# Kernel optimization log

Hardware: AMD Instinct MI355X
Metric: run time of the kernel (lower is better)

Reference implementation:

```python
import jax, jax.numpy as jnp
import numpy as np

HEADS = 8
DIM_HEAD = 64
QUERY_DIM = 1024
CONTEXT_DIM = 768
INNER = HEADS * DIM_HEAD  # 512


def setup_inputs() -> dict:
    key = jax.random.key(0)
    ks = jax.random.split(key, 7)
    B, Sq, Skv = 4, 4096, 1024
    x = jax.random.normal(ks[0], (B, Sq, QUERY_DIM), dtype=jnp.float32)
    context = jax.random.normal(ks[1], (B, Skv, CONTEXT_DIM), dtype=jnp.float32)
    # nn.Linear(in, out) weights stored as [out, in]; we use [in, out] for x @ W
    Wq = jax.random.normal(ks[2], (QUERY_DIM, INNER), dtype=jnp.float32) * (QUERY_DIM ** -0.5)
    Wk = jax.random.normal(ks[3], (CONTEXT_DIM, INNER), dtype=jnp.float32) * (CONTEXT_DIM ** -0.5)
    Wv = jax.random.normal(ks[4], (CONTEXT_DIM, INNER), dtype=jnp.float32) * (CONTEXT_DIM ** -0.5)
    Wo = jax.random.normal(ks[5], (INNER, QUERY_DIM), dtype=jnp.float32) * (INNER ** -0.5)
    bo = jax.random.normal(ks[6], (QUERY_DIM,), dtype=jnp.float32) * 0.01
    return {"x": x, "context": context, "Wq": Wq, "Wk": Wk, "Wv": Wv, "Wo": Wo, "bo": bo}


def reference(x, context, Wq, Wk, Wv, Wo, bo):
    B, Sq, _ = x.shape
    h, d = HEADS, DIM_HEAD
    scale = d ** -0.5
    # project and split heads: [B, S, h*d] -> [B, h, S, d]
    q = (x @ Wq).reshape(B, Sq, h, d).transpose(0, 2, 1, 3)
    k = (context @ Wk).reshape(B, -1, h, d).transpose(0, 2, 1, 3)
    v = (context @ Wv).reshape(B, -1, h, d).transpose(0, 2, 1, 3)
    # the torch chunked loop is exactly full softmax attention (softmax is row-wise)
    scores = jnp.einsum('bhid,bhjd->bhij', q, k) * scale
    attn = jax.nn.softmax(scores, axis=-1)
    out = jnp.einsum('bhij,bhjd->bhid', attn, v)  # [B, h, Sq, d]
    out = out.transpose(0, 2, 1, 3).reshape(B, Sq, h * d)
    return out @ Wo + bo
```

## Files before the change

### kernel.cpp

```cpp
#include <hip/hip_runtime.h>

#define SQ 4096
#define SKV 1024
#define BATCH 4
#define NH 8
#define DH 64
#define QD 1024
#define CD 768
#define INNER 512

typedef _Float16 half8 __attribute__((ext_vector_type(8)));
typedef _Float16 half4v __attribute__((ext_vector_type(4)));
typedef float floatx4 __attribute__((ext_vector_type(4)));
typedef float f32x16 __attribute__((ext_vector_type(16)));
typedef unsigned int uint4v __attribute__((ext_vector_type(4)));

#define MFMA16(a, b, c) __builtin_amdgcn_mfma_f32_16x16x32_f16(a, b, c, 0, 0, 0)
#define MFMA32(a, b, c) __builtin_amdgcn_mfma_f32_32x32x16_f16(a, b, c, 0, 0, 0)

#define PLSWAP(a, b) asm("v_permlane32_swap_b32 %0, %1" : "+v"(a), "+v"(b))

#define GLD16(gptr, lptr)                                                            \
  __builtin_amdgcn_global_load_lds(                                                  \
      (const __attribute__((address_space(1))) unsigned int*)(const void*)(gptr),    \
      (__attribute__((address_space(3))) unsigned int*)(void*)(lptr), 16, 0, 0)

__global__ __launch_bounds__(256) void transpose_all(const float* __restrict__ Wq,
                                                     const float* __restrict__ Wk,
                                                     const float* __restrict__ Wv,
                                                     const float* __restrict__ Wo,
                                                     _Float16* __restrict__ wqt,
                                                     _Float16* __restrict__ wkvt,
                                                     _Float16* __restrict__ wot) {
  __shared__ float tile[32][33];
  const int z = blockIdx.z;
  const float* src; _Float16* dst; int R, C;
  if (z == 0)      { src = Wq; dst = wqt;                        R = QD;    C = INNER; }
  else if (z == 1) { src = Wk; dst = wkvt;                       R = CD;    C = INNER; }
  else if (z == 2) { src = Wv; dst = wkvt + (size_t)INNER * CD;  R = CD;    C = INNER; }
  else             { src = Wo; dst = wot;                        R = INNER; C = QD;   }
  const int c0 = blockIdx.x * 32, r0 = blockIdx.y * 32;
  if (c0 >= C || r0 >= R) return;
  const int tx = threadIdx.x & 31, ty = threadIdx.x >> 5;
#pragma unroll
  for (int i = 0; i < 32; i += 8)
    tile[ty + i][tx] = src[(size_t)(r0 + ty + i) * C + c0 + tx];
  __syncthreads();
#pragma unroll
  for (int i = 0; i < 32; i += 8)
    dst[(size_t)(c0 + ty + i) * R + r0 + tx] = (_Float16)tile[tx][ty + i];
}

template <int MODE, int AF32>
__device__ __forceinline__ void gemm_body(const void* __restrict__ Aany,
                                          const _Float16* __restrict__ Bt,
                                          void* __restrict__ Cout,
                                          void* __restrict__ Cout2,
                                          const float* __restrict__ bias,
                                          int M, int N, int K, int bx, int by,
                                          void* AsRaw, _Float16* Bs) {
  float* As32 = (float*)AsRaw;
  _Float16* As16 = (_Float16*)AsRaw;
  const int tid = threadIdx.x;
  const int wave = tid >> 6, lane = tid & 63;
  const int quad = lane >> 4, l16 = lane & 15;
  const int wm = (wave >> 1) * 64, wn = (wave & 1) * 64;
  const size_t n0 = (size_t)bx * 128, m0 = (size_t)by * 128;

  floatx4 acc[4][4] = {};

  const float* a32g = (const float*)Aany + (m0 + (tid >> 3)) * (size_t)K + (tid & 7) * 4;
  const _Float16* a16g = (const _Float16*)Aany + (m0 + (tid >> 2)) * (size_t)K + (tid & 3) * 8;
  const _Float16* bg = Bt + (n0 + (tid >> 2)) * (size_t)K + (tid & 3) * 8;

#define GSTAGE(bi, k0)                                                        \
  do {                                                                        \
    if (AF32) {                                                               \
      GLD16(a32g + (k0), As32 + (bi)*4096 + tid * 4);                         \
      GLD16(a32g + (k0) + (size_t)32 * K, As32 + (bi)*4096 + tid * 4 + 1024); \
      GLD16(a32g + (k0) + (size_t)64 * K, As32 + (bi)*4096 + tid * 4 + 2048); \
      GLD16(a32g + (k0) + (size_t)96 * K, As32 + (bi)*4096 + tid * 4 + 3072); \
    } else {                                                                  \
      GLD16(a16g + (k0), As16 + (bi)*4096 + tid * 8);                         \
      GLD16(a16g + (k0) + (size_t)64 * K, As16 + (bi)*4096 + tid * 8 + 2048); \
    }                                                                         \
    GLD16(bg + (k0), Bs + (bi)*4096 + tid * 8);                               \
    GLD16(bg + (k0) + (size_t)64 * K, Bs + (bi)*4096 + tid * 8 + 2048);       \
  } while (0)

  const int NT = K / 32;
  GSTAGE(0, 0);
  for (int t = 0; t < NT; ++t) {
    __syncthreads();
    if (t + 1 < NT) GSTAGE((t + 1) & 1, (t + 1) * 32);
    const int bo = (t & 1) * 4096;

    half8 af[4], bf[4];
#pragma unroll
    for (int mt = 0; mt < 4; ++mt) {
      const int row = wm + mt * 16 + l16;
      if (AF32) {
        floatx4 x0 = *(const floatx4*)(As32 + bo + row * 32 + quad * 8);
        floatx4 x1 = *(const floatx4*)(As32 + bo + row * 32 + quad * 8 + 4);
        half8 tt;
#pragma unroll
        for (int i = 0; i < 4; ++i) { tt[i] = (_Float16)x0[i]; tt[4 + i] = (_Float16)x1[i]; }
        af[mt] = tt;
      } else {
        af[mt] = *(const half8*)(As16 + bo + row * 32 + quad * 8);
      }
    }
#pragma unroll
    for (int nt = 0; nt < 4; ++nt)
      bf[nt] = *(const half8*)(Bs + bo + (wn + nt * 16 + l16) * 32 + quad * 8);
    __builtin_amdgcn_s_setprio(1);
#pragma unroll
    for (int mt = 0; mt < 4; ++mt)
#pragma unroll
      for (int nt = 0; nt < 4; ++nt)
        acc[mt][nt] = MFMA16(af[mt], bf[nt], acc[mt][nt]);
    __builtin_amdgcn_s_setprio(0);
  }
#undef GSTAGE

  if (MODE == 3) {
    _Float16* C = (_Float16*)Cout;
    const float sc = 0.125f * 1.44269504088896f;
#pragma unroll
    for (int mt = 0; mt < 4; ++mt) {
      const size_t row = m0 + wm + mt * 16 + quad * 4;
#pragma unroll
      for (int nt = 0; nt < 4; ++nt) {
        const size_t col = n0 + wn + nt * 16 + l16;
#pragma unroll
        for (int r = 0; r < 4; ++r)
          C[(row + r) * N + col] = (_Float16)(acc[mt][nt][r] * sc);
      }
    }
  } else if (MODE == 4) {
    if (n0 < INNER) {
      _Float16* C = (_Float16*)Cout;
#pragma unroll
      for (int mt = 0; mt < 4; ++mt) {
        const size_t row = m0 + wm + mt * 16 + quad * 4;
#pragma unroll
        for (int nt = 0; nt < 4; ++nt) {
          const size_t col = n0 + wn + nt * 16 + l16;
#pragma unroll
          for (int r = 0; r < 4; ++r)
            C[(row + r) * INNER + col] = (_Float16)acc[mt][nt][r];
        }
      }
    } else {
      _Float16* C = (_Float16*)Cout2;
      const int b = (int)(m0 >> 10);
#pragma unroll
      for (int mt = 0; mt < 4; ++mt) {
        const int kvb = (int)(m0 & 1023) + wm + mt * 16 + quad * 4;
#pragma unroll
        for (int nt = 0; nt < 4; ++nt) {
          const int col = (int)(n0 - INNER + wn + nt * 16 + l16);
          const int h = col >> 6, d = col & 63;
          half4v pk;
#pragma unroll
          for (int r = 0; r < 4; ++r) pk[r] = (_Float16)acc[mt][nt][r];
          *(half4v*)(C + (size_t)((b * NH + h) * DH + d) * SKV + kvb) = pk;
        }
      }
    }
  } else {
    float* C = (float*)Cout;
#pragma unroll
    for (int mt = 0; mt < 4; ++mt) {
      const size_t row = m0 + wm + mt * 16 + quad * 4;
#pragma unroll
      for (int nt = 0; nt < 4; ++nt) {
        const size_t col = n0 + wn + nt * 16 + l16;
        const float bb = bias[col];
#pragma unroll
        for (int r = 0; r < 4; ++r)
          C[(row + r) * N + col] = acc[mt][nt][r] + bb;
      }
    }
  }
}

__global__ __launch_bounds__(256) void proj_fused(const float* __restrict__ x,
                                                  const float* __restrict__ ctx,
                                                  const _Float16* __restrict__ wqt,
                                                  const _Float16* __restrict__ wkvt,
                                                  _Float16* __restrict__ qh,
                                                  _Float16* __restrict__ kh,
                                                  _Float16* __restrict__ vth) {
  __shared__ float As32[2 * 128 * 32];
  __shared__ _Float16 Bs[2 * 128 * 32];
  const int b = blockIdx.x;
  const int xcd = b & 7, j = b >> 3;
  const int seg = j % 3;
  if (seg == 2) {
    const int jkv = j / 3;
    gemm_body<4, 1>((const void*)ctx, wkvt, kh, vth, nullptr, BATCH * SKV,
                    2 * INNER, CD, jkv & 7, xcd * 4 + (jkv >> 3), As32, Bs);
  } else {
    const int jq = (j / 3) * 2 + seg;
    gemm_body<3, 1>((const void*)x, wqt, qh, nullptr, nullptr, BATCH * SQ,
                    INNER, QD, jq & 3, xcd * 16 + (jq >> 2), As32, Bs);
  }
}

__global__ __launch_bounds__(256) void gemm_out(const _Float16* __restrict__ A,
                                                const _Float16* __restrict__ Bt,
                                                float* __restrict__ Cout,
                                                const float* __restrict__ bias) {
  __shared__ _Float16 As16[2 * 128 * 32];
  __shared__ _Float16 Bs[2 * 128 * 32];
  const int b = blockIdx.x;
  const int xcd = b & 7, i = b >> 3;
  gemm_body<2, 0>((const void*)A, Bt, Cout, nullptr, bias, BATCH * SQ, QD, INNER,
                  i & 7, xcd * 16 + (i >> 3), As16, Bs);
}

__global__ __launch_bounds__(256, 3) void flash_attn8(const _Float16* __restrict__ Q,
                                                      const _Float16* __restrict__ Kp,
                                                      const _Float16* __restrict__ Vt,
                                                      _Float16* __restrict__ O) {
  __shared__ _Float16 Ksb[2 * 64 * 64];
  __shared__ _Float16 Vsb[2 * 64 * 64];
  const int tid = threadIdx.x;
  const int wave = tid >> 6, lane = tid & 63;
  const int l31 = lane & 31, hi = lane >> 5, x7 = lane & 7;

  const int flat = blockIdx.x;
  const int nf = (flat & 7) * 128 + (flat >> 3);
  const int qblk = nf & 31, bh = nf >> 5;
  const int b = bh >> 3, h = bh & 7;

  const size_t qrow0 = (size_t)b * SQ + qblk * 128 + wave * 32;
  const _Float16* qptr = Q + qrow0 * INNER + h * DH;
  const _Float16* kbase = Kp + (size_t)b * SKV * INNER + h * DH;
  const _Float16* vbase = Vt + (size_t)bh * DH * SKV;

  const int kr = tid >> 3;
  const int kb = (tid & 7) ^ (kr & 7);
  const _Float16* kg = kbase + (size_t)kr * INNER + kb * 8;
  const _Float16* vg = vbase + (size_t)kr * SKV + kb * 8;

#define STAGE_KV(bi, tt)                                                        \
  do {                                                                          \
    _Float16* _kl = Ksb + (bi) * 4096 + tid * 8;                                \
    _Float16* _vl = Vsb + (bi) * 4096 + tid * 8;                                \
    GLD16(kg + (size_t)((tt) * 64) * INNER, _kl);                               \
    GLD16(kg + (size_t)((tt) * 64 + 32) * INNER, _kl + 2048);                   \
    GLD16(vg + (tt) * 64, _vl);                                                 \
    GLD16(vg + (size_t)32 * SKV + (tt) * 64, _vl + 2048);                       \
  } while (0)

  half8 aq[4];
#pragma unroll
  for (int i = 0; i < 4; ++i)
    aq[i] = *(const half8*)(qptr + (size_t)l31 * INNER + i * 16 + hi * 8);

  int koff[4], voffB[4];
#pragma unroll
  for (int i = 0; i < 4; ++i)
    koff[i] = l31 * 64 + (((i * 2 + hi) ^ x7) << 3);
#pragma unroll
  for (int j = 0; j < 4; ++j)
    voffB[j] = l31 * 64 + (((j * 2 + hi) ^ x7) << 3);

  half8 ones;
#pragma unroll
  for (int j = 0; j < 8; ++j) ones[j] = (_Float16)1.0f;

  f32x16 o0 = {}, o1 = {}, osum = {};

  STAGE_KV(0, 0);

  for (int t = 0; t < SKV / 64; ++t) {
    __syncthreads();
    if (t < SKV / 64 - 1) STAGE_KV((t + 1) & 1, t + 1);
    const _Float16* ks = Ksb + (t & 1) * 4096;
    const _Float16* vs = Vsb + (t & 1) * 4096;

#pragma unroll
    for (int c2 = 0; c2 < 2; ++c2) {
      half8 ak[4];
#pragma unroll
      for (int i = 0; i < 4; ++i)
        ak[i] = *(const half8*)(ks + c2 * 2048 + koff[i]);

      f32x16 st = {};
#pragma unroll
      for (int i = 0; i < 4; ++i) st = MFMA32(ak[i], aq[i], st);

      unsigned w[8];
#pragma unroll
      for (int j = 0; j < 8; ++j) {
        float plo = __builtin_exp2f(st[2 * j]);
        float phi = __builtin_exp2f(st[2 * j + 1]);
        w[j] = __builtin_bit_cast(unsigned, __builtin_amdgcn_cvt_pkrtz(plo, phi));
      }
      PLSWAP(w[0], w[2]);
      PLSWAP(w[1], w[3]);
      PLSWAP(w[4], w[6]);
      PLSWAP(w[5], w[7]);
      uint4v u0 = {w[0], w[1], w[2], w[3]};
      uint4v u1 = {w[4], w[5], w[6], w[7]};
      half8 A0 = __builtin_bit_cast(half8, u0);
      half8 A1 = __builtin_bit_cast(half8, u1);

      osum = MFMA32(A0, ones, osum);
      osum = MFMA32(A1, ones, osum);

      {
        half8 bv00 = *(const half8*)(vs + 0 * 2048 + voffB[c2 * 2 + 0]);
        half8 bv10 = *(const half8*)(vs + 1 * 2048 + voffB[c2 * 2 + 0]);
        o0 = MFMA32(A0, bv00, o0);
        o1 = MFMA32(A0, bv10, o1);
        half8 bv01 = *(const half8*)(vs + 0 * 2048 + voffB[c2 * 2 + 1]);
        half8 bv11 = *(const half8*)(vs + 1 * 2048 + voffB[c2 * 2 + 1]);
        o0 = MFMA32(A1, bv01, o0);
        o1 = MFMA32(A1, bv11, o1);
      }
    }
  }

  float inv16[16];
#pragma unroll
  for (int r = 0; r < 16; ++r) inv16[r] = 1.0f / osum[r];

  _Float16* op = O + qrow0 * INNER + h * DH;
#pragma unroll
  for (int r = 0; r < 16; ++r) {
    const int q = (r & 3) + 8 * (r >> 2) + 4 * hi;
    op[(size_t)q * INNER + l31] = (_Float16)(o0[r] * inv16[r]);
    op[(size_t)q * INNER + 32 + l31] = (_Float16)(o1[r] * inv16[r]);
  }
#undef STAGE_KV
}

extern "C" void kernel_launch(void* const* d_in, const int* in_sizes, int n_in,
                              void* d_out, int out_size, void* d_ws, size_t ws_size,
                              hipStream_t stream) {
  const float* x   = (const float*)d_in[0];
  const float* ctx = (const float*)d_in[1];
  const float* Wq  = (const float*)d_in[2];
  const float* Wk  = (const float*)d_in[3];
  const float* Wv  = (const float*)d_in[4];
  const float* Wo  = (const float*)d_in[5];
  const float* bo  = (const float*)d_in[6];
  float* out = (float*)d_out;

  _Float16* ws = (_Float16*)d_ws;
  _Float16* wqt  = ws;
  _Float16* wkvt = wqt + (size_t)INNER * QD;
  _Float16* wot  = wkvt + (size_t)2 * INNER * CD;
  _Float16* qh   = wot + (size_t)QD * INNER;
  _Float16* kh   = qh + (size_t)BATCH * SQ * INNER;
  _Float16* vth  = kh + (size_t)BATCH * SKV * INNER;
  _Float16* aoh  = vth + (size_t)BATCH * SKV * INNER;

  transpose_all<<<dim3(32, 32, 4), 256, 0, stream>>>(Wq, Wk, Wv, Wo, wqt, wkvt, wot);

  proj_fused<<<dim3(768), 256, 0, stream>>>(x, ctx, wqt, wkvt, qh, kh, vth);

  flash_attn8<<<dim3(BATCH * NH * SQ / 128), 256, 0, stream>>>(qh, kh, vth, aoh);

  gemm_out<<<dim3(1024), 256, 0, stream>>>(aoh, wot, out, bo);
}
```

Before: 255.6 us.

## Replace LDS-staged projection GEMMs with direct global-to-register loads

The projection and output GEMMs drop their double-buffered shared-memory staging (global_load_lds plus barriers) and instead load MFMA fragments straight from global memory into registers, unrolling the K loop by two. N and K become template constants, and the launch bounds now request 3 blocks per SM. The aim is to remove LDS traffic and __syncthreads overhead and raise occupancy. In exchange, each wave issues strided, poorly coalesced global loads with no sharing across waves, so it leans heavily on L1/L2 and loses the latency hiding that the explicit double buffer provided.

```diff
diff --git a/kernel.cpp b/kernel.cpp
--- a/kernel.cpp
+++ b/kernel.cpp
@@ -51,16 +51,13 @@
     dst[(size_t)(c0 + ty + i) * R + r0 + tx] = (_Float16)tile[tx][ty + i];
 }
 
-template <int MODE, int AF32>
-__device__ __forceinline__ void gemm_body(const void* __restrict__ Aany,
-                                          const _Float16* __restrict__ Bt,
-                                          void* __restrict__ Cout,
-                                          void* __restrict__ Cout2,
-                                          const float* __restrict__ bias,
-                                          int M, int N, int K, int bx, int by,
-                                          void* AsRaw, _Float16* Bs) {
-  float* As32 = (float*)AsRaw;
-  _Float16* As16 = (_Float16*)AsRaw;
+template <int MODE, int AF32, int N, int K>
+__device__ __forceinline__ void gemm_reg(const void* __restrict__ Aany,
+                                         const _Float16* __restrict__ Bt,
+                                         void* __restrict__ Cout,
+                                         void* __restrict__ Cout2,
+                                         const float* __restrict__ bias,
+                                         int bx, int by) {
   const int tid = threadIdx.x;
   const int wave = tid >> 6, lane = tid & 63;
   const int quad = lane >> 4, l16 = lane & 15;
@@ -69,59 +66,35 @@
 
   floatx4 acc[4][4] = {};
 
-  const float* a32g = (const float*)Aany + (m0 + (tid >> 3)) * (size_t)K + (tid & 7) * 4;
-  const _Float16* a16g = (const _Float16*)Aany + (m0 + (tid >> 2)) * (size_t)K + (tid & 3) * 8;
-  const _Float16* bg = Bt + (n0 + (tid >> 2)) * (size_t)K + (tid & 3) * 8;
-
-#define GSTAGE(bi, k0)                                                        \
-  do {                                                                        \
-    if (AF32) {                                                               \
-      GLD16(a32g + (k0), As32 + (bi)*4096 + tid * 4);                         \
-      GLD16(a32g + (k0) + (size_t)32 * K, As32 + (bi)*4096 + tid * 4 + 1024); \
-      GLD16(a32g + (k0) + (size_t)64 * K, As32 + (bi)*4096 + tid * 4 + 2048); \
-      GLD16(a32g + (k0) + (size_t)96 * K, As32 + (bi)*4096 + tid * 4 + 3072); \
-    } else {                                                                  \
-      GLD16(a16g + (k0), As16 + (bi)*4096 + tid * 8);                         \
-      GLD16(a16g + (k0) + (size_t)64 * K, As16 + (bi)*4096 + tid * 8 + 2048); \
-    }                                                                         \
-    GLD16(bg + (k0), Bs + (bi)*4096 + tid * 8);                               \
-    GLD16(bg + (k0) + (size_t)64 * K, Bs + (bi)*4096 + tid * 8 + 2048);       \
-  } while (0)
-
-  const int NT = K / 32;
-  GSTAGE(0, 0);
-  for (int t = 0; t < NT; ++t) {
-    __syncthreads();
-    if (t + 1 < NT) GSTAGE((t + 1) & 1, (t + 1) * 32);
-    const int bo = (t & 1) * 4096;
-
+  const float* a32 = (const float*)Aany + (m0 + wm + l16) * (size_t)K + quad * 8;
+  const _Float16* a16 = (const _Float16*)Aany + (m0 + wm + l16) * (size_t)K + quad * 8;
+  const _Float16* bg = Bt + (n0 + wn + l16) * (size_t)K + quad * 8;
+
+#pragma unroll 2
+  for (int k0 = 0; k0 < K; k0 += 32) {
     half8 af[4], bf[4];
 #pragma unroll
+    for (int nt = 0; nt < 4; ++nt)
+      bf[nt] = *(const half8*)(bg + (size_t)nt * 16 * K + k0);
+#pragma unroll
     for (int mt = 0; mt < 4; ++mt) {
-      const int row = wm + mt * 16 + l16;
       if (AF32) {
-        floatx4 x0 = *(const floatx4*)(As32 + bo + row * 32 + quad * 8);
-        floatx4 x1 = *(const floatx4*)(As32 + bo + row * 32 + quad * 8 + 4);
+        floatx4 x0 = *(const floatx4*)(a32 + (size_t)mt * 16 * K + k0);
+        floatx4 x1 = *(const floatx4*)(a32 + (size_t)mt * 16 * K + k0 + 4);
         half8 tt;
 #pragma unroll
         for (int i = 0; i < 4; ++i) { tt[i] = (_Float16)x0[i]; tt[4 + i] = (_Float16)x1[i]; }
         af[mt] = tt;
       } else {
-        af[mt] = *(const half8*)(As16 + bo + row * 32 + quad * 8);
-      }
-    }
-#pragma unroll
-    for (int nt = 0; nt < 4; ++nt)
-      bf[nt] = *(const half8*)(Bs + bo + (wn + nt * 16 + l16) * 32 + quad * 8);
-    __builtin_amdgcn_s_setprio(1);
+        af[mt] = *(const half8*)(a16 + (size_t)mt * 16 * K + k0);
+      }
+    }
 #pragma unroll
     for (int mt = 0; mt < 4; ++mt)
 #pragma unroll
       for (int nt = 0; nt < 4; ++nt)
         acc[mt][nt] = MFMA16(af[mt], bf[nt], acc[mt][nt]);
-    __builtin_amdgcn_s_setprio(0);
-  }
-#undef GSTAGE
+  }
 
   if (MODE == 3) {
     _Float16* C = (_Float16*)Cout;
@@ -185,39 +158,35 @@
   }
 }
 
-__global__ __launch_bounds__(256) void proj_fused(const float* __restrict__ x,
-                                                  const float* __restrict__ ctx,
-                                                  const _Float16* __restrict__ wqt,
-                                                  const _Float16* __restrict__ wkvt,
-                                                  _Float16* __restrict__ qh,
-                                                  _Float16* __restrict__ kh,
-                                                  _Float16* __restrict__ vth) {
-  __shared__ float As32[2 * 128 * 32];
-  __shared__ _Float16 Bs[2 * 128 * 32];
+__global__ __launch_bounds__(256, 3) void proj_fused(const float* __restrict__ x,
+                                                     const float* __restrict__ ctx,
+                                                     const _Float16* __restrict__ wqt,
+                                                     const _Float16* __restrict__ wkvt,
+                                                     _Float16* __restrict__ qh,
+                                                     _Float16* __restrict__ kh,
+                                                     _Float16* __restrict__ vth) {
   const int b = blockIdx.x;
   const int xcd = b & 7, j = b >> 3;
   const int seg = j % 3;
   if (seg == 2) {
     const int jkv = j / 3;
-    gemm_body<4, 1>((const void*)ctx, wkvt, kh, vth, nullptr, BATCH * SKV,
-                    2 * INNER, CD, jkv & 7, xcd * 4 + (jkv >> 3), As32, Bs);
+    gemm_reg<4, 1, 2 * INNER, CD>((const void*)ctx, wkvt, kh, vth, nullptr,
+                                  jkv & 7, xcd * 4 + (jkv >> 3));
   } else {
     const int jq = (j / 3) * 2 + seg;
-    gemm_body<3, 1>((const void*)x, wqt, qh, nullptr, nullptr, BATCH * SQ,
-                    INNER, QD, jq & 3, xcd * 16 + (jq >> 2), As32, Bs);
-  }
-}
-
-__global__ __launch_bounds__(256) void gemm_out(const _Float16* __restrict__ A,
-                                                const _Float16* __restrict__ Bt,
-                                                float* __restrict__ Cout,
-                                                const float* __restrict__ bias) {
-  __shared__ _Float16 As16[2 * 128 * 32];
-  __shared__ _Float16 Bs[2 * 128 * 32];
+    gemm_reg<3, 1, INNER, QD>((const void*)x, wqt, qh, nullptr, nullptr,
+                              jq & 3, xcd * 16 + (jq >> 2));
+  }
+}
+
+__global__ __launch_bounds__(256, 3) void gemm_out(const _Float16* __restrict__ A,
+                                                   const _Float16* __restrict__ Bt,
+                                                   float* __restrict__ Cout,
+                                                   const float* __restrict__ bias) {
   const int b = blockIdx.x;
   const int xcd = b & 7, i = b >> 3;
-  gemm_body<2, 0>((const void*)A, Bt, Cout, nullptr, bias, BATCH * SQ, QD, INNER,
-                  i & 7, xcd * 16 + (i >> 3), As16, Bs);
+  gemm_reg<2, 0, QD, INNER>((const void*)A, Bt, Cout, nullptr, bias,
+                            i & 7, xcd * 16 + (i >> 3));
 }
 
 __global__ __launch_bounds__(256, 3) void flash_attn8(const _Float16* __restrict__ Q,
```

Result: slower. 359.4 us (+40.6%).
